# Kernel optimization log

Hardware: AMD Instinct MI355X
Metric: run time of the kernel (lower is better)

## Reference

```python
import jax, jax.numpy as jnp
import numpy as np

CUTOFF = 0.05

def _freq_filter(x_chw, filter_type):
    # x_chw: [C,H,W] = batch element 0, detached in the original (stop_gradient)
    x = jax.lax.stop_gradient(x_chw)
    C, H, W = x.shape
    a = jnp.abs(x)
    mn = a.min(axis=(1, 2), keepdims=True)
    ptp = a.max(axis=(1, 2), keepdims=True) - mn
    # np.uint8(255*(a-mn)/ptp): values in [0,255], cast truncates -> floor
    q = jnp.floor(255.0 * (a - mn) / ptp)
    f = jnp.fft.fftshift(jnp.fft.fft2(q), axes=(-2, -1))
    crow, ccol = H // 2, W // 2
    dr, dc = int(CUTOFF * crow), int(CUTOFF * ccol)
    m = jnp.zeros((H, W), dtype=q.dtype)
    m = m.at[crow - dr:crow + dr, ccol - dc:ccol + dc].set(1.0)
    if filter_type == 'low_pass':
        m = 1.0 - m  # note: original 'low_pass' actually removes low freqs
    out = jnp.abs(jnp.fft.ifft2(jnp.fft.ifftshift(f * m, axes=(-2, -1))))
    return out.astype(x_chw.dtype)  # [C,H,W]

def _conv1x1(x, w, b):
    # x: [B,C,H,W], w: [O,C], b: [O]
    return jnp.einsum('oc,bchw->bohw', w, x) + b[None, :, None, None]

def setup_inputs() -> dict:
    key = jax.random.key(0)
    ks = jax.random.split(key, 7)
    B, C, H, W = 1, 256, 96, 96
    fuse = jax.random.normal(ks[0], (B, C, H, W), dtype=jnp.float32)
    s = 1.0 / np.sqrt(C)
    Wq = jax.random.normal(ks[1], (C, C), dtype=jnp.float32) * s
    bq = jax.random.normal(ks[2], (C,), dtype=jnp.float32) * 0.01
    Wk = jax.random.normal(ks[3], (C, C), dtype=jnp.float32) * s
    bk = jax.random.normal(ks[4], (C,), dtype=jnp.float32) * 0.01
    Wv = jax.random.normal(ks[5], (C, C), dtype=jnp.float32) * s
    bv = jax.random.normal(ks[6], (C,), dtype=jnp.float32) * 0.01
    return {"fuse": fuse, "Wq": Wq, "bq": bq, "Wk": Wk, "bk": bk, "Wv": Wv, "bv": bv}

def reference(fuse, Wq, bq, Wk, bk, Wv, bv):
    B, C, H, W = fuse.shape
    scale = 1.0 / (C ** 0.5)
    # frequency-filtered maps (computed from batch 0, broadcast to all batches)
    FQ = jnp.broadcast_to(_freq_filter(fuse[0], 'high_pass'), fuse.shape)
    FK = jnp.broadcast_to(_freq_filter(fuse[0], 'low_pass'), fuse.shape)
    fuse_Query = _conv1x1(FQ, Wq, bq).reshape(B, C, H * W)     # [B,C,HW]
    fuse_Q_mask = fuse_Query.reshape(B * H, C * W)             # [B*H, C*W]
    fuse_Query_t = jnp.transpose(fuse_Query, (0, 2, 1))        # [B,HW,C]
    fuse_Key = _conv1x1(FK, Wk, bk).reshape(B, C, H * W)       # [B,C,HW]
    Fuse_Q_mask = jnp.max(fuse_Q_mask, axis=0, keepdims=True)  # [1, C*W]
    mask_KQ = jnp.einsum('bnc,bcm->bnm', fuse_Query_t, fuse_Key) * scale  # [B,HW,HW]
    mask_KQ = jax.nn.softmax(mask_KQ, axis=0)  # softmax over batch dim (as in original)
    mask_KQ = jnp.max(mask_KQ, axis=1)                         # [B,HW]
    mask_KQ = mask_KQ.reshape(-1, W)                           # [B*H, W]
    mask_KQ = jnp.max(mask_KQ, axis=-1, keepdims=True)         # [B*H, 1]
    mask = (mask_KQ @ Fuse_Q_mask).reshape(B, C, H, W)
    fuse_Value = _conv1x1(fuse, Wv, bv)
    return fuse_Value + fuse_Value * mask
```

## Files before the change

kernel.cpp:

```cpp
#include <hip/hip_runtime.h>
#include <math.h>

#define CCH 256
#define HW  9216
#define CW  24576
#define TWO_PI 6.28318530717958647692f

typedef __attribute__((ext_vector_type(8))) short short8;
typedef __attribute__((ext_vector_type(4))) float f32x4;

__device__ inline unsigned short f2bf(float f) {
    unsigned u = __float_as_uint(f);
    unsigned r = (u + 0x7FFFu + ((u >> 16) & 1u)) >> 16;
    return (unsigned short)r;
}

__global__ __launch_bounds__(256) void k_front(const float* __restrict__ x,
                                               const float* __restrict__ Wq,
                                               const float* __restrict__ Wv,
                                               short8* __restrict__ Wqt,
                                               short8* __restrict__ Wvt,
                                               unsigned short* __restrict__ XTv,
                                               float* __restrict__ PartLo,
                                               float* __restrict__ PartHi,
                                               unsigned* __restrict__ FQm) {
    __shared__ unsigned short lt[64][66];
    __shared__ float sabs[64][65];
    __shared__ float slo[64][4], shi[64][4];
    int bid = blockIdx.x;
    int t = threadIdx.x;
    if (bid < 576) {
        int ptile = bid % 144, ct = bid / 144;
        int tx = t & 63, tw = t >> 6;
        int p0 = ptile * 64, c0 = ct * 64;
        #pragma unroll
        for (int i = 0; i < 16; ++i) {
            int row = tw * 16 + i;
            float v = x[(size_t)(c0 + row) * HW + p0 + tx];
            lt[row][tx] = f2bf(v);
            sabs[row][tx] = fabsf(v);
        }
        __syncthreads();
        {
            int row = t >> 2, seg = t & 3;
            float lo = sabs[row][seg * 16], hi = lo;
            #pragma unroll
            for (int j = 1; j < 16; ++j) {
                float a = sabs[row][seg * 16 + j];
                lo = fminf(lo, a);
                hi = fmaxf(hi, a);
            }
            slo[row][seg] = lo; shi[row][seg] = hi;
        }
        short8* dst = (short8*)XTv;
        __syncthreads();
        if (t < 64) {
            float lo = fminf(fminf(slo[t][0], slo[t][1]), fminf(slo[t][2], slo[t][3]));
            float hi = fmaxf(fmaxf(shi[t][0], shi[t][1]), fmaxf(shi[t][2], shi[t][3]));
            PartLo[(size_t)(c0 + t) * 144 + ptile] = lo;
            PartHi[(size_t)(c0 + t) * 144 + ptile] = hi;
        }
        #pragma unroll
        for (int ch = 0; ch < 2; ++ch) {
            int lc = ch * 256 + t;
            int kcg = lc >> 6, n = lc & 63;
            short8 v;
            #pragma unroll
            for (int e = 0; e < 8; ++e) v[e] = (short)lt[kcg * 8 + e][n];
            dst[ptile * 2048 + (ct * 8 + kcg) * 64 + n] = v;
        }
    } else {
        int widx = bid - 576;
        int z0 = widx * 384;
        FQm[z0 + t] = 0u;
        if (t < 128) FQm[z0 + 256 + t] = 0u;
        const float* src = (widx >= 32) ? Wv : Wq;
        short8* dst = (widx >= 32) ? Wvt : Wqt;
        int cidx = (widx & 31) * 256 + t;
        int ot = cidx >> 11, kc = (cidx >> 6) & 31, m = cidx & 63;
        const float* s = src + (ot * 64 + m) * 256 + kc * 8;
        short8 v;
        #pragma unroll
        for (int e = 0; e < 8; ++e) v[e] = (short)f2bf(s[e]);
        dst[cidx] = v;
    }
}

__global__ __launch_bounds__(768) void k_dft(const float* __restrict__ x,
                                             const float* __restrict__ PartLo,
                                             const float* __restrict__ PartHi,
                                             float* __restrict__ Fg) {
    __shared__ float cs[96][2];
    __shared__ float Gp[8][96][5];
    __shared__ float Gs[96][6];
    __shared__ float s_mn, s_ptp;
    int c = blockIdx.x, t = threadIdx.x;
    if (t < 96) { float a = TWO_PI * (float)t / 96.0f; cs[t][0] = cosf(a); cs[t][1] = sinf(a); }
    if (t >= 128 && t < 192) {
        int u = t - 128;
        float lo = 1e30f, hi = 0.f;
        for (int i = u; i < 144; i += 64) {
            lo = fminf(lo, PartLo[(size_t)c * 144 + i]);
            hi = fmaxf(hi, PartHi[(size_t)c * 144 + i]);
        }
        #pragma unroll
        for (int d = 32; d; d >>= 1) {
            lo = fminf(lo, __shfl_xor(lo, d, 64));
            hi = fmaxf(hi, __shfl_xor(hi, d, 64));
        }
        if (u == 0) { s_mn = lo; s_ptp = hi - lo; }
    }
    __syncthreads();
    float mn = s_mn, ptp = s_ptp;

    {
        int xx = t % 96, h = t / 96;
        const float* xp = x + c * HW;
        float g0r = 0, g0i = 0, g1r = 0, g1i = 0, g2 = 0;
        for (int y = h * 12; y < h * 12 + 12; ++y) {
            float a = fabsf(xp[y * 96 + xx]);
            float q = floorf(255.0f * (a - mn) / ptp);
            float c1 = cs[y][0], s1 = cs[y][1];
            float c2 = c1 * c1 - s1 * s1, s2 = 2.0f * c1 * s1;
            g0r += q * c2; g0i += q * s2;
            g1r += q * c1; g1i += q * s1;
            g2  += q;
        }
        Gp[h][xx][0] = g0r; Gp[h][xx][1] = g0i;
        Gp[h][xx][2] = g1r; Gp[h][xx][3] = g1i;
        Gp[h][xx][4] = g2;
    }
    __syncthreads();
    if (t < 96) {
        #pragma unroll
        for (int j = 0; j < 5; ++j) {
            float s = 0.f;
            #pragma unroll
            for (int h = 0; h < 8; ++h) s += Gp[h][t][j];
            Gs[t][j] = s;
        }
        Gs[t][5] = 0.f;
    }
    __syncthreads();
    if (t < 64) {
        int coef = t >> 2, qq = t & 3;
        int ky = coef >> 2, kx = coef & 3;
        float fr = 0, fi = 0;
        for (int xx = qq * 24; xx < qq * 24 + 24; ++xx) {
            float c1 = cs[xx][0], s1 = cs[xx][1];
            float er, ei;
            if (kx == 0)      { er = c1 * c1 - s1 * s1; ei = 2.0f * c1 * s1; }
            else if (kx == 1) { er = c1; ei = s1; }
            else if (kx == 2) { er = 1.f; ei = 0.f; }
            else              { er = c1; ei = -s1; }
            float gr, gi;
            if (ky == 0)      { gr = Gs[xx][0]; gi = Gs[xx][1]; }
            else if (ky == 1) { gr = Gs[xx][2]; gi = Gs[xx][3]; }
            else if (ky == 2) { gr = Gs[xx][4]; gi = 0.f; }
            else              { gr = Gs[xx][2]; gi = -Gs[xx][3]; }
            fr += gr * er - gi * ei;
            fi += gr * ei + gi * er;
        }
        fr += __shfl_xor(fr, 1, 64); fr += __shfl_xor(fr, 2, 64);
        fi += __shfl_xor(fi, 1, 64); fi += __shfl_xor(fi, 2, 64);
        if (qq == 0) {
            Fg[c * 32 + 2 * coef]     = fr;
            Fg[c * 32 + 2 * coef + 1] = fi;
        }
    }
}

__global__ __launch_bounds__(256) void k_synth(const float* __restrict__ Fg,
                                               unsigned short* __restrict__ XTq) {
    int c = threadIdx.x;
    int bx = blockIdx.x;
    int y0 = blockIdx.y * 32;
    float Fr[4][4], Fi[4][4];
    #pragma unroll
    for (int k = 0; k < 16; ++k) {
        Fr[k >> 2][k & 3] = Fg[c * 32 + 2 * k];
        Fi[k >> 2][k & 3] = Fg[c * 32 + 2 * k + 1];
    }
    float ax = TWO_PI * (float)bx / 96.0f;
    float cx = cosf(ax), sx = sinf(ax);
    float cx2 = cx * cx - sx * sx, sx2 = 2.0f * cx * sx;
    float Txr[4] = { cx2, cx, 1.f, cx };
    float Txi[4] = { -sx2, -sx, 0.f, sx };
    float Pr[4], Pi[4];
    #pragma unroll
    for (int ky = 0; ky < 4; ++ky) {
        float pr = 0, pi = 0;
        #pragma unroll
        for (int kx = 0; kx < 4; ++kx) {
            pr += Fr[ky][kx] * Txr[kx] - Fi[ky][kx] * Txi[kx];
            pi += Fr[ky][kx] * Txi[kx] + Fi[ky][kx] * Txr[kx];
        }
        Pr[ky] = pr; Pi[ky] = pi;
    }
    const float inv = 1.0f / 9216.0f;
    for (int y = y0; y < y0 + 32; ++y) {
        float ay = TWO_PI * (float)y / 96.0f;
        float cy = cosf(ay), sy = sinf(ay);
        float cy2 = cy * cy - sy * sy, sy2 = 2.0f * cy * sy;
        float ar =  Pr[0] * cy2 + Pi[0] * sy2 + Pr[1] * cy + Pi[1] * sy + Pr[2] + Pr[3] * cy - Pi[3] * sy;
        float ai = -Pr[0] * sy2 + Pi[0] * cy2 - Pr[1] * sy + Pi[1] * cy + Pi[2] + Pr[3] * sy + Pi[3] * cy;
        float v = sqrtf(ar * ar + ai * ai) * inv;
        int p = y * 96 + bx;
        XTq[(size_t)(((p >> 6) * 2048) + ((c >> 3) * 64) + (p & 63)) * 8 + (c & 7)] = f2bf(v);
    }
}

template<int EPI>
__global__ __launch_bounds__(256) void k_gemm(const short8* __restrict__ Wt,
                                              const short8* __restrict__ Xt,
                                              const float* __restrict__ bias,
                                              unsigned* __restrict__ FQm,
                                              float* __restrict__ out) {
    __shared__ short8 As[2048];
    __shared__ short8 Bs[2048];
    int tid = threadIdx.x;
    int pt_ = blockIdx.x, ot = blockIdx.y;
    const short8* wsrc = Wt + ot * 2048;
    const short8* xsrc = Xt + pt_ * 2048;
    #pragma unroll
    for (int i = 0; i < 8; ++i) As[i * 256 + tid] = wsrc[i * 256 + tid];
    #pragma unroll
    for (int i = 0; i < 8; ++i) Bs[i * 256 + tid] = xsrc[i * 256 + tid];
    __syncthreads();

    int l = tid & 63, w = tid >> 6;
    int wr = w >> 1, wc = w & 1;
    int l15 = l & 15, quad = l >> 4;
    f32x4 acc[2][2] = {};
    int abase = wr * 32 + l15;
    int bbase = wc * 32 + l15;
    #pragma unroll
    for (int s = 0; s < 8; ++s) {
        int kc = s * 4 + quad;
        short8 a0 = As[kc * 64 + abase];
        short8 a1 = As[kc * 64 + abase + 16];
        short8 b0 = Bs[kc * 64 + bbase];
        short8 b1 = Bs[kc * 64 + bbase + 16];
        acc[0][0] = __builtin_amdgcn_mfma_f32_16x16x32_bf16(a0, b0, acc[0][0], 0, 0, 0);
        acc[0][1] = __builtin_amdgcn_mfma_f32_16x16x32_bf16(a0, b1, acc[0][1], 0, 0, 0);
        acc[1][0] = __builtin_amdgcn_mfma_f32_16x16x32_bf16(a1, b0, acc[1][0], 0, 0, 0);
        acc[1][1] = __builtin_amdgcn_mfma_f32_16x16x32_bf16(a1, b1, acc[1][1], 0, 0, 0);
    }

    if (EPI == 1) {
        #pragma unroll
        for (int ni = 0; ni < 2; ++ni) {
            #pragma unroll
            for (int r = 0; r < 4; ++r) {
                int o_lo = ot * 64 + wr * 32 + quad * 4 + r;
                float v = fmaxf(acc[0][ni][r] + bias[o_lo], acc[1][ni][r] + bias[o_lo + 16]);
                v = fmaxf(v, __shfl_xor(v, 32, 64));
                if (quad < 2) {
                    int p = pt_ * 64 + wc * 32 + ni * 16 + l15;
                    int k = ((quad * 4 + r) & 7) * HW + p;
                    if (k >= CW) k -= CW;
                    if (k >= CW) k -= CW;
                    unsigned u = __float_as_uint(v);
                    unsigned key = (u & 0x80000000u) ? ~u : (u | 0x80000000u);
                    atomicMax(&FQm[k], key);
                }
            }
        }
    } else {
        #pragma unroll
        for (int mi = 0; mi < 2; ++mi) {
            #pragma unroll
            for (int ni = 0; ni < 2; ++ni) {
                #pragma unroll
                for (int r = 0; r < 4; ++r) {
                    int o = ot * 64 + wr * 32 + mi * 16 + quad * 4 + r;
                    int p = pt_ * 64 + wc * 32 + ni * 16 + l15;
                    int k = ((quad * 4 + r) & 7) * HW + p;
                    if (k >= CW) k -= CW;
                    if (k >= CW) k -= CW;
                    unsigned key = FQm[k];
                    unsigned ub = (key & 0x80000000u) ? (key ^ 0x80000000u) : ~key;
                    float m = __uint_as_float(ub);
                    float v = acc[mi][ni][r] + bias[o];
                    out[(size_t)o * HW + p] = v * (1.0f + m);
                }
            }
        }
    }
}

extern "C" void kernel_launch(void* const* d_in, const int* in_sizes, int n_in,
                              void* d_out, int out_size, void* d_ws, size_t ws_size,
                              hipStream_t stream) {
    const float* fuse = (const float*)d_in[0];
    const float* Wq   = (const float*)d_in[1];
    const float* bq   = (const float*)d_in[2];
    const float* Wv   = (const float*)d_in[5];
    const float* bv   = (const float*)d_in[6];
    float* out = (float*)d_out;

    char* ws = (char*)d_ws;
    unsigned*       FQm    = (unsigned*)(ws);
    float*          Fg     = (float*)(ws + 98304);
    short8*         Wqt    = (short8*)(ws + 131072);
    short8*         Wvt    = (short8*)(ws + 262144);
    float*          PartLo = (float*)(ws + 393216);
    float*          PartHi = (float*)(ws + 540672);
    unsigned short* XTq    = (unsigned short*)(ws + 688128);
    unsigned short* XTv    = (unsigned short*)(ws + 5406720);

    k_front<<<640, 256, 0, stream>>>(fuse, Wq, Wv, Wqt, Wvt, XTv, PartLo, PartHi, FQm);
    k_dft<<<256, 768, 0, stream>>>(fuse, PartLo, PartHi, Fg);
    k_synth<<<dim3(96, 3), 256, 0, stream>>>(Fg, XTq);
    k_gemm<1><<<dim3(144, 4), 256, 0, stream>>>(Wqt, (const short8*)XTq, bq, FQm, nullptr);
    k_gemm<2><<<dim3(144, 4), 256, 0, stream>>>(Wvt, (const short8*)XTv, bv, FQm, out);
}
```

Measured before the change: 117.7 us.

## Fuse inverse-DFT synthesis and input transpose into GEMM prologues

The separate k_synth kernel and the XTq/XTv staging buffers are gone. The first GEMM now rebuilds its filtered B tile on the fly from the 16 retained Fourier coefficients per channel, and the second GEMM converts and transposes the fp32 input into bf16 in shared memory itself. The per-channel min/max reduction moves into k_dft, which caches |x| in LDS, so the PartLo/PartHi partials and the big front kernel are dropped. This saves one launch and several global round trips. In exchange, every GEMM block repeats trig and synthesis work (each of the 4 output-tile blocks recomputes it) and the second GEMM reads fp32 input four times.

```diff
diff --git a/kernel.cpp b/kernel.cpp
--- a/kernel.cpp
+++ b/kernel.cpp
@@ -15,111 +15,67 @@
     return (unsigned short)r;
 }
 
-__global__ __launch_bounds__(256) void k_front(const float* __restrict__ x,
-                                               const float* __restrict__ Wq,
-                                               const float* __restrict__ Wv,
-                                               short8* __restrict__ Wqt,
-                                               short8* __restrict__ Wvt,
-                                               unsigned short* __restrict__ XTv,
-                                               float* __restrict__ PartLo,
-                                               float* __restrict__ PartHi,
-                                               unsigned* __restrict__ FQm) {
-    __shared__ unsigned short lt[64][66];
-    __shared__ float sabs[64][65];
-    __shared__ float slo[64][4], shi[64][4];
-    int bid = blockIdx.x;
+__global__ __launch_bounds__(256) void k_wf(const float* __restrict__ Wq,
+                                            const float* __restrict__ Wv,
+                                            short8* __restrict__ Wqt,
+                                            short8* __restrict__ Wvt,
+                                            unsigned* __restrict__ FQm) {
+    int widx = blockIdx.x;
     int t = threadIdx.x;
-    if (bid < 576) {
-        int ptile = bid % 144, ct = bid / 144;
-        int tx = t & 63, tw = t >> 6;
-        int p0 = ptile * 64, c0 = ct * 64;
-        #pragma unroll
-        for (int i = 0; i < 16; ++i) {
-            int row = tw * 16 + i;
-            float v = x[(size_t)(c0 + row) * HW + p0 + tx];
-            lt[row][tx] = f2bf(v);
-            sabs[row][tx] = fabsf(v);
-        }
-        __syncthreads();
-        {
-            int row = t >> 2, seg = t & 3;
-            float lo = sabs[row][seg * 16], hi = lo;
-            #pragma unroll
-            for (int j = 1; j < 16; ++j) {
-                float a = sabs[row][seg * 16 + j];
-                lo = fminf(lo, a);
-                hi = fmaxf(hi, a);
-            }
-            slo[row][seg] = lo; shi[row][seg] = hi;
-        }
-        short8* dst = (short8*)XTv;
-        __syncthreads();
-        if (t < 64) {
-            float lo = fminf(fminf(slo[t][0], slo[t][1]), fminf(slo[t][2], slo[t][3]));
-            float hi = fmaxf(fmaxf(shi[t][0], shi[t][1]), fmaxf(shi[t][2], shi[t][3]));
-            PartLo[(size_t)(c0 + t) * 144 + ptile] = lo;
-            PartHi[(size_t)(c0 + t) * 144 + ptile] = hi;
-        }
-        #pragma unroll
-        for (int ch = 0; ch < 2; ++ch) {
-            int lc = ch * 256 + t;
-            int kcg = lc >> 6, n = lc & 63;
-            short8 v;
-            #pragma unroll
-            for (int e = 0; e < 8; ++e) v[e] = (short)lt[kcg * 8 + e][n];
-            dst[ptile * 2048 + (ct * 8 + kcg) * 64 + n] = v;
-        }
-    } else {
-        int widx = bid - 576;
-        int z0 = widx * 384;
-        FQm[z0 + t] = 0u;
-        if (t < 128) FQm[z0 + 256 + t] = 0u;
-        const float* src = (widx >= 32) ? Wv : Wq;
-        short8* dst = (widx >= 32) ? Wvt : Wqt;
-        int cidx = (widx & 31) * 256 + t;
-        int ot = cidx >> 11, kc = (cidx >> 6) & 31, m = cidx & 63;
-        const float* s = src + (ot * 64 + m) * 256 + kc * 8;
-        short8 v;
-        #pragma unroll
-        for (int e = 0; e < 8; ++e) v[e] = (short)f2bf(s[e]);
-        dst[cidx] = v;
-    }
+    int z0 = widx * 384;
+    FQm[z0 + t] = 0u;
+    if (t < 128) FQm[z0 + 256 + t] = 0u;
+    const float* src = (widx >= 32) ? Wv : Wq;
+    short8* dst = (widx >= 32) ? Wvt : Wqt;
+    int cidx = (widx & 31) * 256 + t;
+    int ot = cidx >> 11, kc = (cidx >> 6) & 31, m = cidx & 63;
+    const float* s = src + (ot * 64 + m) * 256 + kc * 8;
+    short8 v;
+    #pragma unroll
+    for (int e = 0; e < 8; ++e) v[e] = (short)f2bf(s[e]);
+    dst[cidx] = v;
 }
 
 __global__ __launch_bounds__(768) void k_dft(const float* __restrict__ x,
-                                             const float* __restrict__ PartLo,
-                                             const float* __restrict__ PartHi,
                                              float* __restrict__ Fg) {
+    __shared__ float qa[HW];
     __shared__ float cs[96][2];
     __shared__ float Gp[8][96][5];
     __shared__ float Gs[96][6];
+    __shared__ float red[24];
     __shared__ float s_mn, s_ptp;
     int c = blockIdx.x, t = threadIdx.x;
+    const float* xp = x + c * HW;
     if (t < 96) { float a = TWO_PI * (float)t / 96.0f; cs[t][0] = cosf(a); cs[t][1] = sinf(a); }
-    if (t >= 128 && t < 192) {
-        int u = t - 128;
-        float lo = 1e30f, hi = 0.f;
-        for (int i = u; i < 144; i += 64) {
-            lo = fminf(lo, PartLo[(size_t)c * 144 + i]);
-            hi = fmaxf(hi, PartHi[(size_t)c * 144 + i]);
-        }
-        #pragma unroll
-        for (int d = 32; d; d >>= 1) {
-            lo = fminf(lo, __shfl_xor(lo, d, 64));
-            hi = fmaxf(hi, __shfl_xor(hi, d, 64));
-        }
-        if (u == 0) { s_mn = lo; s_ptp = hi - lo; }
+    float lo = 1e30f, hi = 0.f;
+    #pragma unroll
+    for (int i = 0; i < 12; ++i) {
+        float a = fabsf(xp[t + i * 768]);
+        qa[t + i * 768] = a;
+        lo = fminf(lo, a);
+        hi = fmaxf(hi, a);
+    }
+    #pragma unroll
+    for (int d = 32; d; d >>= 1) {
+        lo = fminf(lo, __shfl_xor(lo, d, 64));
+        hi = fmaxf(hi, __shfl_xor(hi, d, 64));
+    }
+    if ((t & 63) == 0) { red[t >> 6] = lo; red[12 + (t >> 6)] = hi; }
+    __syncthreads();
+    if (t == 0) {
+        lo = red[0]; hi = red[12];
+        #pragma unroll
+        for (int i = 1; i < 12; ++i) { lo = fminf(lo, red[i]); hi = fmaxf(hi, red[12 + i]); }
+        s_mn = lo; s_ptp = hi - lo;
     }
     __syncthreads();
     float mn = s_mn, ptp = s_ptp;
 
     {
         int xx = t % 96, h = t / 96;
-        const float* xp = x + c * HW;
         float g0r = 0, g0i = 0, g1r = 0, g1i = 0, g2 = 0;
         for (int y = h * 12; y < h * 12 + 12; ++y) {
-            float a = fabsf(xp[y * 96 + xx]);
-            float q = floorf(255.0f * (a - mn) / ptp);
+            float q = floorf(255.0f * (qa[y * 96 + xx] - mn) / ptp);
             float c1 = cs[y][0], s1 = cs[y][1];
             float c2 = c1 * c1 - s1 * s1, s2 = 2.0f * c1 * s1;
             g0r += q * c2; g0i += q * s2;
@@ -170,62 +126,72 @@
     }
 }
 
-__global__ __launch_bounds__(256) void k_synth(const float* __restrict__ Fg,
-                                               unsigned short* __restrict__ XTq) {
-    int c = threadIdx.x;
-    int bx = blockIdx.x;
-    int y0 = blockIdx.y * 32;
-    float Fr[4][4], Fi[4][4];
-    #pragma unroll
-    for (int k = 0; k < 16; ++k) {
-        Fr[k >> 2][k & 3] = Fg[c * 32 + 2 * k];
-        Fi[k >> 2][k & 3] = Fg[c * 32 + 2 * k + 1];
-    }
-    float ax = TWO_PI * (float)bx / 96.0f;
-    float cx = cosf(ax), sx = sinf(ax);
-    float cx2 = cx * cx - sx * sx, sx2 = 2.0f * cx * sx;
-    float Txr[4] = { cx2, cx, 1.f, cx };
-    float Txi[4] = { -sx2, -sx, 0.f, sx };
-    float Pr[4], Pi[4];
-    #pragma unroll
-    for (int ky = 0; ky < 4; ++ky) {
-        float pr = 0, pi = 0;
-        #pragma unroll
-        for (int kx = 0; kx < 4; ++kx) {
-            pr += Fr[ky][kx] * Txr[kx] - Fi[ky][kx] * Txi[kx];
-            pi += Fr[ky][kx] * Txi[kx] + Fi[ky][kx] * Txr[kx];
-        }
-        Pr[ky] = pr; Pi[ky] = pi;
-    }
-    const float inv = 1.0f / 9216.0f;
-    for (int y = y0; y < y0 + 32; ++y) {
-        float ay = TWO_PI * (float)y / 96.0f;
-        float cy = cosf(ay), sy = sinf(ay);
-        float cy2 = cy * cy - sy * sy, sy2 = 2.0f * cy * sy;
-        float ar =  Pr[0] * cy2 + Pi[0] * sy2 + Pr[1] * cy + Pi[1] * sy + Pr[2] + Pr[3] * cy - Pi[3] * sy;
-        float ai = -Pr[0] * sy2 + Pi[0] * cy2 - Pr[1] * sy + Pi[1] * cy + Pi[2] + Pr[3] * sy + Pi[3] * cy;
-        float v = sqrtf(ar * ar + ai * ai) * inv;
-        int p = y * 96 + bx;
-        XTq[(size_t)(((p >> 6) * 2048) + ((c >> 3) * 64) + (p & 63)) * 8 + (c & 7)] = f2bf(v);
-    }
-}
-
-template<int EPI>
-__global__ __launch_bounds__(256) void k_gemm(const short8* __restrict__ Wt,
-                                              const short8* __restrict__ Xt,
-                                              const float* __restrict__ bias,
-                                              unsigned* __restrict__ FQm,
-                                              float* __restrict__ out) {
+__global__ __launch_bounds__(256) void k_gemm1(const short8* __restrict__ Wt,
+                                               const float* __restrict__ Fg,
+                                               const float* __restrict__ bias,
+                                               unsigned* __restrict__ FQm) {
     __shared__ short8 As[2048];
     __shared__ short8 Bs[2048];
+    __shared__ float Rs[2048][2];
     int tid = threadIdx.x;
     int pt_ = blockIdx.x, ot = blockIdx.y;
     const short8* wsrc = Wt + ot * 2048;
-    const short8* xsrc = Xt + pt_ * 2048;
     #pragma unroll
     for (int i = 0; i < 8; ++i) As[i * 256 + tid] = wsrc[i * 256 + tid];
-    #pragma unroll
-    for (int i = 0; i < 8; ++i) Bs[i * 256 + tid] = xsrc[i * 256 + tid];
+
+    int p0 = pt_ * 64;
+    int y0 = p0 / 96;
+    {
+        int yi = (tid >> 2) & 1, kx = tid & 3, cb = tid >> 3;
+        float ay = TWO_PI * (float)(y0 + yi) / 96.0f;
+        float cyv = cosf(ay), syv = sinf(ay);
+        float cy2 = cyv * cyv - syv * syv, sy2 = 2.f * cyv * syv;
+        float Ur[4] = { cy2, cyv, 1.f, cyv };
+        float Ui[4] = { -sy2, -syv, 0.f, syv };
+        #pragma unroll
+        for (int i = 0; i < 8; ++i) {
+            int cc = cb + i * 32;
+            float rr = 0.f, ri = 0.f;
+            #pragma unroll
+            for (int ky = 0; ky < 4; ++ky) {
+                float fr = Fg[cc * 32 + 2 * (ky * 4 + kx)];
+                float fi = Fg[cc * 32 + 2 * (ky * 4 + kx) + 1];
+                rr += fr * Ur[ky] - fi * Ui[ky];
+                ri += fr * Ui[ky] + fi * Ur[ky];
+            }
+            Rs[cc * 8 + yi * 4 + kx][0] = rr;
+            Rs[cc * 8 + yi * 4 + kx][1] = ri;
+        }
+    }
+    __syncthreads();
+    const float inv = 1.0f / 9216.0f;
+    #pragma unroll
+    for (int i = 0; i < 8; ++i) {
+        int si = i * 256 + tid;
+        int kcg = si >> 6, n = si & 63;
+        int p = p0 + n;
+        int y = p / 96, xx = p - y * 96;
+        int yi = y - y0;
+        float axv = TWO_PI * (float)xx / 96.0f;
+        float cxv = cosf(axv), sxv = sinf(axv);
+        float cx2 = cxv * cxv - sxv * sxv, sx2 = 2.f * cxv * sxv;
+        float Tr[4] = { cx2, cxv, 1.f, cxv };
+        float Ti[4] = { -sx2, -sxv, 0.f, sxv };
+        short8 vv;
+        #pragma unroll
+        for (int e = 0; e < 8; ++e) {
+            int rb = (kcg * 8 + e) * 8 + yi * 4;
+            float ar = 0.f, ai = 0.f;
+            #pragma unroll
+            for (int kx = 0; kx < 4; ++kx) {
+                float rr = Rs[rb + kx][0], ri = Rs[rb + kx][1];
+                ar += rr * Tr[kx] - ri * Ti[kx];
+                ai += rr * Ti[kx] + ri * Tr[kx];
+            }
+            vv[e] = (short)f2bf(sqrtf(ar * ar + ai * ai) * inv);
+        }
+        Bs[si] = vv;
+    }
     __syncthreads();
 
     int l = tid & 63, w = tid >> 6;
@@ -246,44 +212,95 @@
         acc[1][0] = __builtin_amdgcn_mfma_f32_16x16x32_bf16(a1, b0, acc[1][0], 0, 0, 0);
         acc[1][1] = __builtin_amdgcn_mfma_f32_16x16x32_bf16(a1, b1, acc[1][1], 0, 0, 0);
     }
-
-    if (EPI == 1) {
+    #pragma unroll
+    for (int ni = 0; ni < 2; ++ni) {
+        #pragma unroll
+        for (int r = 0; r < 4; ++r) {
+            int o_lo = ot * 64 + wr * 32 + quad * 4 + r;
+            float v = fmaxf(acc[0][ni][r] + bias[o_lo], acc[1][ni][r] + bias[o_lo + 16]);
+            v = fmaxf(v, __shfl_xor(v, 32, 64));
+            if (quad < 2) {
+                int p = pt_ * 64 + wc * 32 + ni * 16 + l15;
+                int k = ((quad * 4 + r) & 7) * HW + p;
+                if (k >= CW) k -= CW;
+                if (k >= CW) k -= CW;
+                unsigned u = __float_as_uint(v);
+                unsigned key = (u & 0x80000000u) ? ~u : (u | 0x80000000u);
+                atomicMax(&FQm[k], key);
+            }
+        }
+    }
+}
+
+__global__ __launch_bounds__(256) void k_gemm2(const short8* __restrict__ Wt,
+                                               const float* __restrict__ x,
+                                               const float* __restrict__ bias,
+                                               const unsigned* __restrict__ FQm,
+                                               float* __restrict__ out) {
+    __shared__ short8 As[2048];
+    __shared__ short8 Bs[2048];
+    __shared__ unsigned short lt[64][66];
+    int tid = threadIdx.x;
+    int pt_ = blockIdx.x, ot = blockIdx.y;
+    const short8* wsrc = Wt + ot * 2048;
+    #pragma unroll
+    for (int i = 0; i < 8; ++i) As[i * 256 + tid] = wsrc[i * 256 + tid];
+
+    int p0 = pt_ * 64;
+    int tx = tid & 63, tw = tid >> 6;
+    for (int ct4 = 0; ct4 < 4; ++ct4) {
+        #pragma unroll
+        for (int i = 0; i < 16; ++i) {
+            int row = tw * 16 + i;
+            lt[row][tx] = f2bf(x[(size_t)(ct4 * 64 + row) * HW + p0 + tx]);
+        }
+        __syncthreads();
+        #pragma unroll
+        for (int ch = 0; ch < 2; ++ch) {
+            int lc = ch * 256 + tid;
+            int kcg = lc >> 6, n = lc & 63;
+            short8 v;
+            #pragma unroll
+            for (int e = 0; e < 8; ++e) v[e] = (short)lt[kcg * 8 + e][n];
+            Bs[(ct4 * 8 + kcg) * 64 + n] = v;
+        }
+        __syncthreads();
+    }
+
+    int l = tid & 63, w = tid >> 6;
+    int wr = w >> 1, wc = w & 1;
+    int l15 = l & 15, quad = l >> 4;
+    f32x4 acc[2][2] = {};
+    int abase = wr * 32 + l15;
+    int bbase = wc * 32 + l15;
+    #pragma unroll
+    for (int s = 0; s < 8; ++s) {
+        int kc = s * 4 + quad;
+        short8 a0 = As[kc * 64 + abase];
+        short8 a1 = As[kc * 64 + abase + 16];
+        short8 b0 = Bs[kc * 64 + bbase];
+        short8 b1 = Bs[kc * 64 + bbase + 16];
+        acc[0][0] = __builtin_amdgcn_mfma_f32_16x16x32_bf16(a0, b0, acc[0][0], 0, 0, 0);
+        acc[0][1] = __builtin_amdgcn_mfma_f32_16x16x32_bf16(a0, b1, acc[0][1], 0, 0, 0);
+        acc[1][0] = __builtin_amdgcn_mfma_f32_16x16x32_bf16(a1, b0, acc[1][0], 0, 0, 0);
+        acc[1][1] = __builtin_amdgcn_mfma_f32_16x16x32_bf16(a1, b1, acc[1][1], 0, 0, 0);
+    }
+    #pragma unroll
+    for (int mi = 0; mi < 2; ++mi) {
         #pragma unroll
         for (int ni = 0; ni < 2; ++ni) {
             #pragma unroll
             for (int r = 0; r < 4; ++r) {
-                int o_lo = ot * 64 + wr * 32 + quad * 4 + r;
-                float v = fmaxf(acc[0][ni][r] + bias[o_lo], acc[1][ni][r] + bias[o_lo + 16]);
-                v = fmaxf(v, __shfl_xor(v, 32, 64));
-                if (quad < 2) {
-                    int p = pt_ * 64 + wc * 32 + ni * 16 + l15;
-                    int k = ((quad * 4 + r) & 7) * HW + p;
-                    if (k >= CW) k -= CW;
-                    if (k >= CW) k -= CW;
-                    unsigned u = __float_as_uint(v);
-                    unsigned key = (u & 0x80000000u) ? ~u : (u | 0x80000000u);
-                    atomicMax(&FQm[k], key);
-                }
-            }
-        }
-    } else {
-        #pragma unroll
-        for (int mi = 0; mi < 2; ++mi) {
-            #pragma unroll
-            for (int ni = 0; ni < 2; ++ni) {
-                #pragma unroll
-                for (int r = 0; r < 4; ++r) {
-                    int o = ot * 64 + wr * 32 + mi * 16 + quad * 4 + r;
-                    int p = pt_ * 64 + wc * 32 + ni * 16 + l15;
-                    int k = ((quad * 4 + r) & 7) * HW + p;
-                    if (k >= CW) k -= CW;
-                    if (k >= CW) k -= CW;
-                    unsigned key = FQm[k];
-                    unsigned ub = (key & 0x80000000u) ? (key ^ 0x80000000u) : ~key;
-                    float m = __uint_as_float(ub);
-                    float v = acc[mi][ni][r] + bias[o];
-                    out[(size_t)o * HW + p] = v * (1.0f + m);
-                }
+                int o = ot * 64 + wr * 32 + mi * 16 + quad * 4 + r;
+                int p = pt_ * 64 + wc * 32 + ni * 16 + l15;
+                int k = ((quad * 4 + r) & 7) * HW + p;
+                if (k >= CW) k -= CW;
+                if (k >= CW) k -= CW;
+                unsigned key = FQm[k];
+                unsigned ub = (key & 0x80000000u) ? (key ^ 0x80000000u) : ~key;
+                float m = __uint_as_float(ub);
+                float v = acc[mi][ni][r] + bias[o];
+                out[(size_t)o * HW + p] = v * (1.0f + m);
             }
         }
     }
@@ -300,18 +317,13 @@
     float* out = (float*)d_out;
 
     char* ws = (char*)d_ws;
-    unsigned*       FQm    = (unsigned*)(ws);
-    float*          Fg     = (float*)(ws + 98304);
-    short8*         Wqt    = (short8*)(ws + 131072);
-    short8*         Wvt    = (short8*)(ws + 262144);
-    float*          PartLo = (float*)(ws + 393216);
-    float*          PartHi = (float*)(ws + 540672);
-    unsigned short* XTq    = (unsigned short*)(ws + 688128);
-    unsigned short* XTv    = (unsigned short*)(ws + 5406720);
-
-    k_front<<<640, 256, 0, stream>>>(fuse, Wq, Wv, Wqt, Wvt, XTv, PartLo, PartHi, FQm);
-    k_dft<<<256, 768, 0, stream>>>(fuse, PartLo, PartHi, Fg);
-    k_synth<<<dim3(96, 3), 256, 0, stream>>>(Fg, XTq);
-    k_gemm<1><<<dim3(144, 4), 256, 0, stream>>>(Wqt, (const short8*)XTq, bq, FQm, nullptr);
-    k_gemm<2><<<dim3(144, 4), 256, 0, stream>>>(Wvt, (const short8*)XTv, bv, FQm, out);
-}
+    unsigned* FQm = (unsigned*)(ws);
+    float*    Fg  = (float*)(ws + 98304);
+    short8*   Wqt = (short8*)(ws + 131072);
+    short8*   Wvt = (short8*)(ws + 262144);
+
+    k_wf<<<64, 256, 0, stream>>>(Wq, Wv, Wqt, Wvt, FQm);
+    k_dft<<<256, 768, 0, stream>>>(fuse, Fg);
+    k_gemm1<<<dim3(144, 4), 256, 0, stream>>>(Wqt, Fg, bq, FQm);
+    k_gemm2<<<dim3(144, 4), 256, 0, stream>>>(Wvt, fuse, bv, FQm, out);
+}
```

New measurement: 120.1 us. No clear change (+2.0%).
